# Performance work log

Measured on AMD Instinct MI355X. Metric: run time of the kernel, lower is better.

Reference implementation:

```python
import jax, jax.numpy as jnp
import numpy as np

R = 3           # disp_range = (3, 3)
DU = 2 * R + 1  # 7 displacements per axis, 49 total
PNAMES = ['mn_w1','mn_b1','mn_w2','mn_b2','mn_w3','mn_b3','mn_w4','mn_b4','mn_wd','mn_bd','mn_w5','mn_b5','dap_w','dap_b','me_w1','me_b1','me_w2','me_b2','me_w3','me_b3','gz1_w','gz1_b','gr1_w','gr1_b','gq1_w','gq1_b','gz2_w','gz2_b','gr2_w','gr2_b','gq2_w','gq2_b','fh_w1','fh_b1','fh_w2','fh_b2']


def conv2d(x, w, b, stride=(1, 1), padding=((1, 1), (1, 1))):
    y = jax.lax.conv_general_dilated(x, w, stride, padding, dimension_numbers=('NCHW', 'OIHW', 'NCHW'))
    return y + b[None, :, None, None]


def warp_backwards(f, flow):
    # bilinear backward warp with zero padding; flow[:,0]=u (x offset), flow[:,1]=v (y offset)
    B, C, H, W = f.shape
    gy, gx = jnp.meshgrid(jnp.arange(H, dtype=flow.dtype), jnp.arange(W, dtype=flow.dtype), indexing='ij')
    x = gx[None] + flow[:, 0]
    y = gy[None] + flow[:, 1]
    x0, y0 = jnp.floor(x), jnp.floor(y)
    wx, wy = x - x0, y - y0

    def corner(yy, xx, wgt):
        valid = (yy >= 0) & (yy <= H - 1) & (xx >= 0) & (xx <= W - 1)
        yc = jnp.clip(yy, 0, H - 1).astype(jnp.int32)
        xc = jnp.clip(xx, 0, W - 1).astype(jnp.int32)
        g = jax.vmap(lambda fb, yb, xb: fb[:, yb, xb])(f, yc, xc)  # (B,C,H,W)
        return g * (wgt * valid.astype(f.dtype))[:, None]

    return (corner(y0, x0, (1 - wy) * (1 - wx)) + corner(y0, x0 + 1, (1 - wy) * wx)
            + corner(y0 + 1, x0, wy * (1 - wx)) + corner(y0 + 1, x0 + 1, wy * wx))


def gru_step(h, x, wz, bz, wr, br, wq, bq, pad):
    hx = jnp.concatenate([h, x], axis=1)
    z = jax.nn.sigmoid(conv2d(hx, wz, bz, padding=pad))
    r = jax.nn.sigmoid(conv2d(hx, wr, br, padding=pad))
    q = jnp.tanh(conv2d(jnp.concatenate([r * h, x], axis=1), wq, bq, padding=pad))
    return (1.0 - z) * h + z * q


def _run(fmap1, fmap2, h, flow, P):
    B, C, H, W = fmap1.shape
    lrelu, relu = jax.nn.leaky_relu, jax.nn.relu
    # backward warp of fmap2 by current (detached) flow
    f2w = warp_backwards(fmap2, jax.lax.stop_gradient(flow))
    # --- correlation volume: 49 zero-padded shifts of warped fmap2, paired with fmap1 ---
    pad2 = jnp.pad(f2w, ((0, 0), (0, 0), (R, R), (R, R)))
    # k = i*DU + j  <->  shift (di, dj) = (i-R, j-R); shifted[...,y,x] = f2w[y+dj, x+di]
    shifted = jnp.stack([pad2[:, :, j:j + H, i:i + W] for i in range(DU) for j in range(DU)], axis=1)  # (B,49,C,H,W)
    valid = (jnp.sum(shifted, axis=2, keepdims=True) != 0).astype(fmap1.dtype)
    mvol = jnp.concatenate([jnp.broadcast_to(fmap1[:, None], shifted.shape), shifted], axis=2) * valid  # (B,49,2C,H,W)
    # --- matching net, applied per displacement ---
    x = mvol.reshape(B * DU * DU, 2 * C, H, W)
    x = relu(conv2d(x, P['mn_w1'], P['mn_b1']))
    x = relu(conv2d(x, P['mn_w2'], P['mn_b2'], stride=(2, 2)))
    x = relu(conv2d(x, P['mn_w3'], P['mn_b3']))
    x = relu(conv2d(x, P['mn_w4'], P['mn_b4']))
    # ConvTranspose2d(k=4, s=2, p=1) == lhs-dilated conv with pad 2
    x = jax.lax.conv_general_dilated(x, P['mn_wd'], (1, 1), ((2, 2), (2, 2)), lhs_dilation=(2, 2), dimension_numbers=('NCHW', 'OIHW', 'NCHW')) + P['mn_bd'][None, :, None, None]
    x = relu(x)
    x = conv2d(x, P['mn_w5'], P['mn_b5'])  # (B*49, 1, H, W)
    cvol = x.reshape(B, DU * DU, H, W)
    # --- displacement-aware projection: 1x1 conv across the 49 displacement channels ---
    cvol = jnp.einsum('ok,bkhw->bohw', P['dap_w'], cvol) + P['dap_b'][None, :, None, None]
    # --- motion encoder ---
    m = jnp.concatenate([cvol, fmap1, flow], axis=1)  # (B, 49+C+2, H, W)
    m = lrelu(conv2d(m, P['me_w1'], P['me_b1']))
    m = lrelu(conv2d(m, P['me_w2'], P['me_b2']))
    m = conv2d(m, P['me_w3'], P['me_b3'])             # (B, 94, H, W)
    xg = jnp.concatenate([m, flow], axis=1)           # (B, 96, H, W)
    # --- separable conv GRU: horizontal (1x5) then vertical (5x1) pass ---
    h = gru_step(h, xg, P['gz1_w'], P['gz1_b'], P['gr1_w'], P['gr1_b'], P['gq1_w'], P['gq1_b'], ((0, 0), (2, 2)))
    h = gru_step(h, xg, P['gz2_w'], P['gz2_b'], P['gr2_w'], P['gr2_b'], P['gq2_w'], P['gq2_b'], ((2, 2), (0, 0)))
    # --- flow head: softmax over 49 displacements, expectation of displacement grid ---
    s = lrelu(jnp.einsum('oi,bihw->bohw', P['fh_w1'], h) + P['fh_b1'][None, :, None, None])
    s = lrelu(jnp.einsum('oi,bihw->bohw', P['fh_w2'], s) + P['fh_b2'][None, :, None, None])
    prob = jax.nn.softmax(s, axis=1)  # (B, 49, H, W)
    dr = jnp.arange(-R, R + 1, dtype=fmap1.dtype)
    disp = jnp.stack([jnp.broadcast_to(dr[:, None], (DU, DU)), jnp.broadcast_to(dr[None, :], (DU, DU))], axis=0).reshape(2, DU * DU)
    d = jnp.einsum('bkhw,ck->bchw', prob, disp)
    return h, flow + d


def _params(key):
    shapes = {'mn_w1': (96, 64, 3, 3), 'mn_b1': (96,), 'mn_w2': (128, 96, 3, 3), 'mn_b2': (128,), 'mn_w3': (128, 128, 3, 3), 'mn_b3': (128,), 'mn_w4': (64, 128, 3, 3), 'mn_b4': (64,), 'mn_wd': (32, 64, 4, 4), 'mn_bd': (32,), 'mn_w5': (1, 32, 3, 3), 'mn_b5': (1,), 'dap_w': (49, 49), 'dap_b': (49,), 'me_w1': (128, 83, 3, 3), 'me_b1': (128,), 'me_w2': (128, 128, 3, 3), 'me_b2': (128,), 'me_w3': (94, 128, 3, 3), 'me_b3': (94,), 'gz1_w': (128, 224, 1, 5), 'gz1_b': (128,), 'gr1_w': (128, 224, 1, 5), 'gr1_b': (128,), 'gq1_w': (128, 224, 1, 5), 'gq1_b': (128,), 'gz2_w': (128, 224, 5, 1), 'gz2_b': (128,), 'gr2_w': (128, 224, 5, 1), 'gr2_b': (128,), 'gq2_w': (128, 224, 5, 1), 'gq2_b': (128,), 'fh_w1': (256, 128), 'fh_b1': (256,), 'fh_w2': (49, 256), 'fh_b2': (49,)}
    keys = jax.random.split(key, len(shapes))
    return {n: jax.random.normal(k, s, dtype=jnp.float32) * 0.05 for (n, s), k in zip(shapes.items(), keys)}


def setup_inputs():
    key = jax.random.key(0)
    k1, k2, k3, k4, kp = jax.random.split(key, 5)
    B, C, H, W, HID = 2, 32, 64, 96, 128
    inp = {'fmap1': jax.random.normal(k1, (B, C, H, W), jnp.float32),
           'fmap2': jax.random.normal(k2, (B, C, H, W), jnp.float32),
           'h': jax.random.normal(k3, (B, HID, H, W), jnp.float32),
           'flow': jax.random.normal(k4, (B, 2, H, W), jnp.float32),
           'i': 0}
    inp.update(_params(kp))
    return inp


def reference(fmap1, fmap2, h, flow, mn_w1, mn_b1, mn_w2, mn_b2, mn_w3, mn_b3, mn_w4, mn_b4, mn_wd, mn_bd, mn_w5, mn_b5, dap_w, dap_b, me_w1, me_b1, me_w2, me_b2, me_w3, me_b3, gz1_w, gz1_b, gr1_w, gr1_b, gq1_w, gq1_b, gz2_w, gz2_b, gr2_w, gr2_b, gq2_w, gq2_b, fh_w1, fh_b1, fh_w2, fh_b2, i):
    ps = (mn_w1, mn_b1, mn_w2, mn_b2, mn_w3, mn_b3, mn_w4, mn_b4, mn_wd, mn_bd, mn_w5, mn_b5, dap_w, dap_b, me_w1, me_b1, me_w2, me_b2, me_w3, me_b3, gz1_w, gz1_b, gr1_w, gr1_b, gq1_w, gq1_b, gz2_w, gz2_b, gr2_w, gr2_b, gq2_w, gq2_b, fh_w1, fh_b1, fh_w2, fh_b2)
    return _run(fmap1, fmap2, h, flow, dict(zip(PNAMES, ps)))
```

## Files before the change

### kernel.cpp

```cpp
#include <hip/hip_runtime.h>
#include <math.h>

typedef unsigned short u16;
typedef unsigned int u32;
typedef __attribute__((ext_vector_type(8))) short bf16x8;
typedef __attribute__((ext_vector_type(4))) float f32x4;

#define HWW 6144

__device__ __forceinline__ float sigmoidf_(float x) { return 1.f / (1.f + expf(-x)); }
__device__ __forceinline__ float lrelu_(float x) { return x >= 0.f ? x : 0.01f * x; }
__device__ __forceinline__ u16 f2bf(float f) {
    u32 u = __float_as_uint(f);
    u += 0x7fffu + ((u >> 16) & 1u);
    return (u16)(u >> 16);
}
__device__ __forceinline__ float bf2f(u16 h) { return __uint_as_float(((u32)h) << 16); }
__device__ __forceinline__ u32 pk2(float a, float b) { return (u32)f2bf(a) | ((u32)f2bf(b) << 16); }

struct WJob { const float* src; unsigned long dstOff; int OC, rowOff, IC, ICP, NT; unsigned long cum; };
struct WJobs { WJob j[16]; long total; };

__global__ __launch_bounds__(256) void k_wt_all(WJobs J, u16* __restrict__ base)
{
    long i = (long)blockIdx.x * 256 + threadIdx.x;
    if (i >= J.total) return;
    int jb = 0;
    #pragma unroll
    for (int k = 1; k < 16; ++k) if (i >= (long)J.j[k].cum) jb = k;
    WJob w = J.j[jb];
    long local = i - (long)w.cum;
    int c = (int)(local % w.ICP);
    int t = (int)((local / w.ICP) % w.NT);
    int o = (int)(local / ((long)w.ICP * w.NT));
    float val = (c < w.IC) ? w.src[((long)o * w.IC + c) * w.NT + t] : 0.f;
    base[w.dstOff + ((long)(w.rowOff + o) * w.NT + t) * w.ICP + c] = f2bf(val);
}

__global__ __launch_bounds__(256) void k_wt_dq(const float* __restrict__ w, u16* __restrict__ dst)
{
    int i = blockIdx.x * 256 + threadIdx.x;
    if (i >= 32768) return;
    int c = i & 63; int t = (i >> 6) & 3; int o = (i >> 8) & 31; int q = i >> 13;
    int ry = q >> 1, rx = q & 1, ta = t >> 1, tb = t & 1;
    int ky = ry + 2 * ta, kx = rx + 2 * tb;
    float val = w[(((long)o * 64 + c) * 4 + ky) * 4 + kx];
    dst[(long)q * 8192 + o * 256 + t * 64 + c] = f2bf(val);
}

__global__ __launch_bounds__(256) void k_wt5(const float* __restrict__ w, float* __restrict__ wt)
{
    int i = blockIdx.x * 256 + threadIdx.x;
    if (i >= 288) return;
    int t = i % 9, c = i / 9;
    wt[t * 32 + c] = w[c * 9 + t];
}

__global__ void k_catb(const float* __restrict__ a, const float* __restrict__ b, float* __restrict__ d)
{
    int i = threadIdx.x;
    if (i < 128) d[i] = a[i];
    else if (i < 256) d[i] = b[i - 128];
}

__global__ __launch_bounds__(256) void k_prep_f1(const float* __restrict__ fmap1, u16* __restrict__ f1bf)
{
    int gid = blockIdx.x * 256 + threadIdx.x;
    if (gid >= 24576) return;
    int idx = gid >> 1, half = gid & 1;
    int b = idx / HWW, p = idx % HWW;
    const float* fb = fmap1 + (long)b * 32 * HWW + p + (long)(half * 16) * HWW;
    u32 pk[8];
    #pragma unroll
    for (int c2 = 0; c2 < 8; ++c2)
        pk[c2] = pk2(fb[(long)(2 * c2) * HWW], fb[(long)(2 * c2 + 1) * HWW]);
    u16* op = f1bf + ((long)idx << 5) + half * 16;
    ((uint4*)op)[0] = make_uint4(pk[0], pk[1], pk[2], pk[3]);
    ((uint4*)op)[1] = make_uint4(pk[4], pk[5], pk[6], pk[7]);
}

__global__ __launch_bounds__(256) void k_warp(const float* __restrict__ fmap2, const float* __restrict__ flow,
                                              u16* __restrict__ f2wbf, float* __restrict__ cs)
{
    int gid = blockIdx.x * 256 + threadIdx.x;
    if (gid >= 24576) return;
    int idx = gid >> 1, half = gid & 1;
    int b = idx / HWW, p = idx % HWW, y = p / 96, x = p % 96;
    float u = flow[(b * 2 + 0) * HWW + p], v = flow[(b * 2 + 1) * HWW + p];
    float fx = (float)x + u, fy = (float)y + v;
    float fx0 = floorf(fx), fy0 = floorf(fy);
    float wx = fx - fx0, wy = fy - fy0;
    int x0 = (int)fx0, y0i = (int)fy0, x1 = x0 + 1, y1 = y0i + 1;
    bool vx0 = x0 >= 0 && x0 < 96, vx1 = x1 >= 0 && x1 < 96;
    bool vy0 = y0i >= 0 && y0i < 64, vy1 = y1 >= 0 && y1 < 64;
    float m00 = (vy0 && vx0) ? (1.f - wy) * (1.f - wx) : 0.f;
    float m01 = (vy0 && vx1) ? (1.f - wy) * wx : 0.f;
    float m10 = (vy1 && vx0) ? wy * (1.f - wx) : 0.f;
    float m11 = (vy1 && vx1) ? wy * wx : 0.f;
    int cx0 = min(max(x0, 0), 95), cx1 = min(max(x1, 0), 95);
    int cy0 = min(max(y0i, 0), 63), cy1 = min(max(y1, 0), 63);
    int i00 = cy0 * 96 + cx0, i01 = cy0 * 96 + cx1, i10 = cy1 * 96 + cx0, i11 = cy1 * 96 + cx1;
    const float* fb = fmap2 + (long)b * 32 * HWW + (long)(half * 16) * HWW;
    float s = 0.f; u32 pk[8];
    #pragma unroll
    for (int c2 = 0; c2 < 8; ++c2) {
        const float* fa = fb + (long)(2 * c2) * HWW;
        const float* fc = fb + (long)(2 * c2 + 1) * HWW;
        float g0 = m00 * fa[i00] + m01 * fa[i01] + m10 * fa[i10] + m11 * fa[i11];
        float g1 = m00 * fc[i00] + m01 * fc[i01] + m10 * fc[i10] + m11 * fc[i11];
        s += g0 + g1;
        pk[c2] = pk2(g0, g1);
    }
    u16* op = f2wbf + ((long)idx << 5) + half * 16;
    ((uint4*)op)[0] = make_uint4(pk[0], pk[1], pk[2], pk[3]);
    ((uint4*)op)[1] = make_uint4(pk[4], pk[5], pk[6], pk[7]);
    float stot = s + __shfl_xor(s, 1);
    if (half == 0) cs[idx] = stot;
}

template<int BM, int BN, int MODE, int KH, int KW, int PH, int PW, int STRIDE, int ACT, int OUTF32,
         int IH, int IW, int OH, int OW, int ICP, int NKT>
__global__ __launch_bounds__(256) void k_gemm(
    const u16* __restrict__ A0, const u16* __restrict__ A1,
    const float* __restrict__ csm, const u16* __restrict__ Wb,
    const float* __restrict__ bias,
    u16* __restrict__ outb, u16* __restrict__ outb2, float* __restrict__ outf,
    int OC, int ldc, int coff, int nOff)
{
    constexpr int WAVES_M = (BM == 64) ? 2 : ((BN == 128) ? 2 : 4);
    constexpr int WAVES_N = 4 / WAVES_M;
    constexpr int WTM = BM / WAVES_M;
    constexpr int WTN = BN / WAVES_N;
    constexpr int MF = WTM / 16;
    constexpr int NF = WTN / 16;
    constexpr int LDR = 40;
    __shared__ u16 As[2][BM * LDR];
    __shared__ u16 Bs[2][BN * LDR];
    int tid = threadIdx.x;
    constexpr int ATHR = 256 / BM;
    int mrow = tid / ATHR;
    int khOff = (tid % ATHR) * (32 / ATHR);
    int gmS = blockIdx.x * BM + mrow;

    constexpr int OHW = (MODE == 1) ? 6144 : ((MODE == 2) ? 1536 : OH * OW);
    constexpr int OWW = (MODE == 1) ? 96 : ((MODE == 2) ? 48 : OW);
    int nImg = gmS / OHW;
    int rem = gmS - nImg * OHW;
    int y0 = rem / OWW, x0 = rem - y0 * OWW;

    int ryz = 0, rxz = 0, diS = 0, djS = 0, bImgHWW = 0;
    u32 vmask = 0;
    const u16* Arow = A0;
    if (MODE == 0) {
        Arow = A0 + ((long)nImg * IH * IW + (long)y0 * STRIDE * IW + (long)x0 * STRIDE) * ICP + khOff;
    } else if (MODE == 1) {
        int n = nOff + nImg;
        int bImg = n / 49; int kd = n - bImg * 49;
        diS = kd / 7 - 3; djS = kd % 7 - 3;
        bImgHWW = bImg * HWW;
        #pragma unroll
        for (int t = 0; t < 9; ++t) {
            int dy = t / 3 - 1, dx = t % 3 - 1;
            int yy = y0 + dy, xx = x0 + dx, ys = yy + djS, xs = xx + diS;
            bool v = yy >= 0 && yy < 64 && xx >= 0 && xx < 96 && ys >= 0 && ys < 64 && xs >= 0 && xs < 96;
            if (v) v = (csm[bImgHWW + ys * 96 + xs] != 0.f);
            vmask |= (v ? 1u : 0u) << t;
        }
    } else {
        ryz = blockIdx.z >> 1; rxz = blockIdx.z & 1;
    }
    const u16* WbZ = Wb + (MODE == 2 ? (long)blockIdx.z * 32 * 256 : 0);
    int n0 = blockIdx.y * BN;

    auto loadTile = [&](int kt, uint4& va0, uint4& va1) {
        va0 = make_uint4(0u, 0u, 0u, 0u); va1 = make_uint4(0u, 0u, 0u, 0u);
        if (MODE == 0) {
            constexpr int KTC = ICP / 32;
            int t = kt / KTC;
            int c0 = (kt - t * KTC) << 5;
            int dy = t / KW - PH, dx = t - (t / KW) * KW - PW;
            int iy = y0 * STRIDE + dy, ix = x0 * STRIDE + dx;
            if (iy >= 0 && iy < IH && ix >= 0 && ix < IW) {
                const u16* sp = Arow + (long)(dy * IW + dx) * ICP + c0;
                va0 = *(const uint4*)sp;
                if (BM == 128) va1 = *(const uint4*)(sp + 8);
            }
        } else if (MODE == 1) {
            int t = kt >> 1, half = kt & 1;
            if ((vmask >> t) & 1u) {
                int dy = t / 3 - 1, dx = t % 3 - 1;
                int yy = y0 + dy, xx = x0 + dx;
                const u16* sp = half ? (A1 + (((long)bImgHWW + (yy + djS) * 96 + (xx + diS)) << 5) + khOff)
                                     : (A0 + (((long)bImgHWW + yy * 96 + xx) << 5) + khOff);
                va0 = *(const uint4*)sp;
                if (BM == 128) va1 = *(const uint4*)(sp + 8);
            }
        } else {
            int t = kt >> 1, c0 = (kt & 1) << 5;
            int ta = t >> 1, tb = t & 1;
            int iy = y0 + ryz + ta - 1, ix = x0 + rxz + tb - 1;
            if (iy >= 0 && iy < 32 && ix >= 0 && ix < 48) {
                const u16* sp = A0 + (((long)(nImg * 32 + iy) * 48 + ix) << 6) + c0 + khOff;
                va0 = *(const uint4*)sp;
                if (BM == 128) va1 = *(const uint4*)(sp + 8);
            }
        }
    };
    auto writeA = [&](int bufn, const uint4& va0, const uint4& va1) {
        *(uint4*)&As[bufn][mrow * LDR + khOff] = va0;
        if (BM == 128) *(uint4*)&As[bufn][mrow * LDR + khOff + 8] = va1;
    };

    bool bldr = (tid < 2 * BN);
    int brow = tid >> 1, ko = (tid & 1) << 4;
    const u16* Bp = WbZ + (long)(n0 + brow) * (NKT * 32) + ko;
    auto loadB = [&](int kt, uint4& vb0, uint4& vb1) {
        const u16* wp = Bp + (long)kt * 32;
        vb0 = *(const uint4*)wp; vb1 = *(const uint4*)(wp + 8);
    };
    auto writeB = [&](int bufn, const uint4& vb0, const uint4& vb1) {
        *(uint4*)&Bs[bufn][brow * LDR + ko] = vb0;
        *(uint4*)&Bs[bufn][brow * LDR + ko + 8] = vb1;
    };

    int lane = tid & 63, wid = tid >> 6;
    int wm = (WAVES_N == 2) ? (wid >> 1) : wid;
    int wn = (WAVES_N == 2) ? (wid & 1) : 0;
    int fr = lane & 15, fg = lane >> 4;
    f32x4 acc[MF][NF];
    #pragma unroll
    for (int i = 0; i < MF; ++i)
        #pragma unroll
        for (int j = 0; j < NF; ++j)
            acc[i][j] = (f32x4){0.f, 0.f, 0.f, 0.f};

    uint4 pa0, pa1, pb0, pb1;
    {
        uint4 t0, t1;
        loadTile(0, t0, t1);
        writeA(0, t0, t1);
        if (bldr) { uint4 u0, u1; loadB(0, u0, u1); writeB(0, u0, u1); }
    }
    if (NKT > 1) {
        loadTile(1, pa0, pa1);
        if (bldr) loadB(1, pb0, pb1);
    }
    __syncthreads();

    #pragma unroll
    for (int kt = 0; kt < NKT; ++kt) {
        int cur = kt & 1;
        uint4 qa0, qa1, qb0, qb1;
        if (kt + 2 < NKT) {
            loadTile(kt + 2, qa0, qa1);
            if (bldr) loadB(kt + 2, qb0, qb1);
        }
        bf16x8 af[MF], bfv[NF];
        #pragma unroll
        for (int i = 0; i < MF; ++i)
            af[i] = *(const bf16x8*)&As[cur][(wm * WTM + i * 16 + fr) * LDR + fg * 8];
        #pragma unroll
        for (int j = 0; j < NF; ++j)
            bfv[j] = *(const bf16x8*)&Bs[cur][(wn * WTN + j * 16 + fr) * LDR + fg * 8];
        #pragma unroll
        for (int i = 0; i < MF; ++i)
            #pragma unroll
            for (int j = 0; j < NF; ++j)
                acc[i][j] = __builtin_amdgcn_mfma_f32_16x16x32_bf16(af[i], bfv[j], acc[i][j], 0, 0, 0);
        if (kt + 1 < NKT) {
            int bufn = cur ^ 1;
            writeA(bufn, pa0, pa1);
            if (bldr) writeB(bufn, pb0, pb1);
            __syncthreads();
            pa0 = qa0; pa1 = qa1; pb0 = qb0; pb1 = qb1;
        }
    }

    #pragma unroll
    for (int i = 0; i < MF; ++i) {
        #pragma unroll
        for (int j = 0; j < NF; ++j) {
            int nn = n0 + wn * WTN + j * 16 + fr;
            if (nn >= OC) continue;
            #pragma unroll
            for (int rr = 0; rr < 4; ++rr) {
                int mloc = wm * WTM + i * 16 + fg * 4 + rr;
                long gm = (long)blockIdx.x * BM + mloc;
                float v = acc[i][j][rr] + bias[nn];
                if (ACT == 1) v = fmaxf(v, 0.f);
                else if (ACT == 2) v = lrelu_(v);
                if (OUTF32) {
                    outf[gm * ldc + coff + nn] = v;
                } else if (MODE == 2) {
                    int nI = (int)(gm / 1536); int rq = (int)(gm - (long)nI * 1536);
                    int Y = rq / 48, X = rq - (rq / 48) * 48;
                    long di = (((long)nI * 64 + 2 * Y + ryz) * 96 + (2 * X + rxz)) * 32 + nn;
                    outb[di] = f2bf(v);
                } else {
                    long di = gm * ldc + coff + nn;
                    u16 hv = f2bf(v);
                    outb[di] = hv;
                    if (outb2) outb2[di] = hv;
                }
            }
        }
    }
}

__global__ __launch_bounds__(256) void k_conv5n(const u16* __restrict__ x5, const float* __restrict__ w5t,
                                                const float* __restrict__ b5, u16* __restrict__ cvolT,
                                                int N, int n0)
{
    int idx = blockIdx.x * 256 + threadIdx.x;
    if (idx >= N * HWW) return;
    int nl = idx / HWW, p = idx % HWW, y = p / 96, x = p % 96;
    float acc = b5[0];
    #pragma unroll
    for (int t = 0; t < 9; ++t) {
        int iy = y + t / 3 - 1, ix = x + t % 3 - 1;
        if (iy < 0 || iy >= 64 || ix < 0 || ix >= 96) continue;
        const u16* sp = x5 + (((long)nl * HWW + iy * 96 + ix) << 5);
        const float* wt_ = w5t + t * 32;
        #pragma unroll
        for (int c8 = 0; c8 < 4; ++c8) {
            uint4 v = *(const uint4*)(sp + c8 * 8);
            acc = fmaf(bf2f((u16)(v.x & 0xffffu)), wt_[c8 * 8 + 0], acc);
            acc = fmaf(bf2f((u16)(v.x >> 16)),     wt_[c8 * 8 + 1], acc);
            acc = fmaf(bf2f((u16)(v.y & 0xffffu)), wt_[c8 * 8 + 2], acc);
            acc = fmaf(bf2f((u16)(v.y >> 16)),     wt_[c8 * 8 + 3], acc);
            acc = fmaf(bf2f((u16)(v.z & 0xffffu)), wt_[c8 * 8 + 4], acc);
            acc = fmaf(bf2f((u16)(v.z >> 16)),     wt_[c8 * 8 + 5], acc);
            acc = fmaf(bf2f((u16)(v.w & 0xffffu)), wt_[c8 * 8 + 6], acc);
            acc = fmaf(bf2f((u16)(v.w >> 16)),     wt_[c8 * 8 + 7], acc);
        }
    }
    int n = n0 + nl;
    int b = n / 49, k = n - b * 49;
    cvolT[((long)b * HWW + p) * 64 + k] = f2bf(acc);
}

__global__ __launch_bounds__(256) void k_me_tail(const float* __restrict__ fmap1, const float* __restrict__ flow,
                                                 u16* __restrict__ mein)
{
    int gid = blockIdx.x * 256 + threadIdx.x;
    if (gid >= 73728) return;
    int j = gid / 12288, idx = gid - j * 12288;
    int b = idx / HWW, p = idx % HWW;
    int c0 = 49 + j * 8;
    u16* mp = mein + (long)idx * 96;
    #pragma unroll
    for (int q = 0; q < 8; ++q) {
        int c = c0 + q;
        if (c >= 96) break;
        float v;
        if (c < 81) v = fmap1[((long)(b * 32 + (c - 49))) * HWW + p];
        else if (c == 81) v = flow[(b * 2 + 0) * HWW + p];
        else if (c == 82) v = flow[(b * 2 + 1) * HWW + p];
        else v = 0.f;
        mp[c] = f2bf(v);
    }
}

__global__ __launch_bounds__(256) void k_set_head(const float* __restrict__ h, const float* __restrict__ flow,
                                                  float* __restrict__ hst, u16* __restrict__ hx,
                                                  u16* __restrict__ hx2)
{
    int gid = blockIdx.x * 256 + threadIdx.x;
    if (gid >= 49152) return;
    int cq = gid / 12288, idx = gid - cq * 12288;
    int b = idx / HWW, p = idx % HWW;
    int c0 = cq * 32;
    const float* hp = h + (long)b * 128 * HWW + p;
    float* hs = hst + (long)idx * 128;
    u16* hxp = hx + (long)idx * 224;
    #pragma unroll
    for (int c = c0; c < c0 + 32; c += 8) {
        float v[8];
        #pragma unroll
        for (int q = 0; q < 8; ++q) v[q] = hp[(long)(c + q) * HWW];
        *(float4*)&hs[c] = make_float4(v[0], v[1], v[2], v[3]);
        *(float4*)&hs[c + 4] = make_float4(v[4], v[5], v[6], v[7]);
        uint4 pk = make_uint4(pk2(v[0], v[1]), pk2(v[2], v[3]), pk2(v[4], v[5]), pk2(v[6], v[7]));
        *(uint4*)&hxp[c] = pk;
    }
    if (cq == 0) {
        u16 uu = f2bf(flow[(b * 2 + 0) * HWW + p]);
        u16 vv = f2bf(flow[(b * 2 + 1) * HWW + p]);
        long o = (long)idx * 224;
        hx[o + 222] = uu; hx[o + 223] = vv;
        hx2[o + 222] = uu; hx2[o + 223] = vv;
    }
}

__global__ __launch_bounds__(256) void k_post_zr(const float* __restrict__ azr, const float* __restrict__ hst,
                                                 float* __restrict__ z, u16* __restrict__ hx2)
{
    int gid = blockIdx.x * 256 + threadIdx.x;
    if (gid >= 49152) return;
    int cq = gid / 12288, idx = gid - cq * 12288;
    int c0 = cq * 32;
    const float* ap = azr + (long)idx * 256;
    const float* hs = hst + (long)idx * 128;
    float* zp = z + (long)idx * 128;
    u16* xp = hx2 + (long)idx * 224;
    #pragma unroll
    for (int c = c0; c < c0 + 32; c += 8) {
        float4 a0 = *(const float4*)&ap[c], a1 = *(const float4*)&ap[c + 4];
        float4 r0 = *(const float4*)&ap[128 + c], r1 = *(const float4*)&ap[128 + c + 4];
        float4 h0 = *(const float4*)&hs[c], h1v = *(const float4*)&hs[c + 4];
        float z0 = sigmoidf_(a0.x), z1 = sigmoidf_(a0.y), z2 = sigmoidf_(a0.z), z3 = sigmoidf_(a0.w);
        float z4 = sigmoidf_(a1.x), z5 = sigmoidf_(a1.y), z6 = sigmoidf_(a1.z), z7 = sigmoidf_(a1.w);
        *(float4*)&zp[c] = make_float4(z0, z1, z2, z3);
        *(float4*)&zp[c + 4] = make_float4(z4, z5, z6, z7);
        float rh0 = sigmoidf_(r0.x) * h0.x, rh1 = sigmoidf_(r0.y) * h0.y;
        float rh2 = sigmoidf_(r0.z) * h0.z, rh3 = sigmoidf_(r0.w) * h0.w;
        float rh4 = sigmoidf_(r1.x) * h1v.x, rh5 = sigmoidf_(r1.y) * h1v.y;
        float rh6 = sigmoidf_(r1.z) * h1v.z, rh7 = sigmoidf_(r1.w) * h1v.w;
        uint4 pk = make_uint4(pk2(rh0, rh1), pk2(rh2, rh3), pk2(rh4, rh5), pk2(rh6, rh7));
        *(uint4*)&xp[c] = pk;
    }
}

template<int FIN>
__global__ __launch_bounds__(256) void k_post_q(const float* __restrict__ aq, const float* __restrict__ z,
                                                const float* __restrict__ hst, float* __restrict__ h1f,
                                                u16* __restrict__ hxdst, float* __restrict__ outH)
{
    int gid = blockIdx.x * 256 + threadIdx.x;
    if (gid >= 49152) return;
    int cq = gid / 12288, idx = gid - cq * 12288;
    int b = idx / HWW, p = idx % HWW;
    int c0 = cq * 32;
    const float* ap = aq + (long)idx * 128;
    const float* zp = z + (long)idx * 128;
    const float* hs = hst + (long)idx * 128;
    #pragma unroll
    for (int c = c0; c < c0 + 32; c += 8) {
        float hn[8];
        #pragma unroll
        for (int q = 0; q < 8; ++q) {
            float qq = tanhf(ap[c + q]);
            float zv = zp[c + q];
            hn[q] = (1.f - zv) * hs[c + q] + zv * qq;
        }
        uint4 pk = make_uint4(pk2(hn[0], hn[1]), pk2(hn[2], hn[3]), pk2(hn[4], hn[5]), pk2(hn[6], hn[7]));
        if (FIN == 0) {
            *(float4*)&h1f[(long)idx * 128 + c] = make_float4(hn[0], hn[1], hn[2], hn[3]);
            *(float4*)&h1f[(long)idx * 128 + c + 4] = make_float4(hn[4], hn[5], hn[6], hn[7]);
            *(uint4*)&hxdst[(long)idx * 224 + c] = pk;
        } else {
            #pragma unroll
            for (int q = 0; q < 8; ++q)
                outH[((long)(b * 128 + c + q)) * HWW + p] = hn[q];
            *(uint4*)&hxdst[(long)idx * 128 + c] = pk;
        }
    }
}

__global__ __launch_bounds__(256) void k_soft(const float* __restrict__ s2, const float* __restrict__ flow,
                                              float* __restrict__ outFlow)
{
    int idx = blockIdx.x * 256 + threadIdx.x;
    if (idx >= 12288) return;
    int b = idx / HWW, p = idx % HWW;
    const float* sp = s2 + (long)idx * 64;
    float lg[49];
    #pragma unroll
    for (int k = 0; k < 48; k += 4) {
        float4 v = *(const float4*)&sp[k];
        lg[k] = v.x; lg[k + 1] = v.y; lg[k + 2] = v.z; lg[k + 3] = v.w;
    }
    lg[48] = sp[48];
    float m = -1e30f;
    #pragma unroll
    for (int k = 0; k < 49; ++k) m = fmaxf(m, lg[k]);
    float s = 0.f, a0 = 0.f, a1 = 0.f;
    #pragma unroll
    for (int k = 0; k < 49; ++k) {
        float e = expf(lg[k] - m);
        s += e;
        a0 += e * (float)(k / 7 - 3);
        a1 += e * (float)(k % 7 - 3);
    }
    float inv = 1.f / s;
    outFlow[(long)(b * 2 + 0) * HWW + p] = flow[(long)(b * 2 + 0) * HWW + p] + a0 * inv;
    outFlow[(long)(b * 2 + 1) * HWW + p] = flow[(long)(b * 2 + 1) * HWW + p] + a1 * inv;
}

extern "C" void kernel_launch(void* const* d_in, const int* in_sizes, int n_in,
                              void* d_out, int out_size, void* d_ws, size_t ws_size,
                              hipStream_t stream)
{
    const float* fmap1 = (const float*)d_in[0];
    const float* fmap2 = (const float*)d_in[1];
    const float* h     = (const float*)d_in[2];
    const float* flow  = (const float*)d_in[3];
    int pb = (in_sizes[4] == 1) ? 5 : 4;
    const float* mn_w1 = (const float*)d_in[pb + 0];
    const float* mn_b1 = (const float*)d_in[pb + 1];
    const float* mn_w2 = (const float*)d_in[pb + 2];
    const float* mn_b2 = (const float*)d_in[pb + 3];
    const float* mn_w3 = (const float*)d_in[pb + 4];
    const float* mn_b3 = (const float*)d_in[pb + 5];
    const float* mn_w4 = (const float*)d_in[pb + 6];
    const float* mn_b4 = (const float*)d_in[pb + 7];
    const float* mn_wd = (const float*)d_in[pb + 8];
    const float* mn_bd = (const float*)d_in[pb + 9];
    const float* mn_w5 = (const float*)d_in[pb + 10];
    const float* mn_b5 = (const float*)d_in[pb + 11];
    const float* dap_w = (const float*)d_in[pb + 12];
    const float* dap_b = (const float*)d_in[pb + 13];
    const float* me_w1 = (const float*)d_in[pb + 14];
    const float* me_b1 = (const float*)d_in[pb + 15];
    const float* me_w2 = (const float*)d_in[pb + 16];
    const float* me_b2 = (const float*)d_in[pb + 17];
    const float* me_w3 = (const float*)d_in[pb + 18];
    const float* me_b3 = (const float*)d_in[pb + 19];
    const float* gz1_w = (const float*)d_in[pb + 20];
    const float* gz1_b = (const float*)d_in[pb + 21];
    const float* gr1_w = (const float*)d_in[pb + 22];
    const float* gr1_b = (const float*)d_in[pb + 23];
    const float* gq1_w = (const float*)d_in[pb + 24];
    const float* gq1_b = (const float*)d_in[pb + 25];
    const float* gz2_w = (const float*)d_in[pb + 26];
    const float* gz2_b = (const float*)d_in[pb + 27];
    const float* gr2_w = (const float*)d_in[pb + 28];
    const float* gr2_b = (const float*)d_in[pb + 29];
    const float* gq2_w = (const float*)d_in[pb + 30];
    const float* gq2_b = (const float*)d_in[pb + 31];
    const float* fh_w1 = (const float*)d_in[pb + 32];
    const float* fh_b1 = (const float*)d_in[pb + 33];
    const float* fh_w2 = (const float*)d_in[pb + 34];
    const float* fh_b2 = (const float*)d_in[pb + 35];

    char* wsB = (char*)d_ws;
    size_t off = 0;
    auto alc = [&](size_t bytes) { size_t o = off; off = (off + bytes + 255) & ~(size_t)255; return o; };

    size_t o_wc1  = alc(128 * 576 * 2);
    size_t o_wc2  = alc(128 * 864 * 2);
    size_t o_wc3  = alc((size_t)128 * 1152 * 2);
    size_t o_wc4  = alc((size_t)64 * 1152 * 2);
    size_t o_wdq  = alc(32768 * 2);
    size_t o_wme1 = alc(128 * 864 * 2);
    size_t o_wme2 = alc((size_t)128 * 1152 * 2);
    size_t o_wme3 = alc((size_t)128 * 1152 * 2);
    size_t o_wzr1 = alc((size_t)256 * 1120 * 2);
    size_t o_wq1  = alc((size_t)128 * 1120 * 2);
    size_t o_wzr2 = alc((size_t)256 * 1120 * 2);
    size_t o_wq2  = alc((size_t)128 * 1120 * 2);
    size_t o_wfh1 = alc(256 * 128 * 2);
    size_t o_wfh2 = alc(64 * 256 * 2);
    size_t o_wdapb= alc(64 * 64 * 2);
    size_t o_w5t  = alc(288 * 4);
    size_t o_bzr1 = alc(256 * 4);
    size_t o_bzr2 = alc(256 * 4);
    size_t wArenaBytes = off;

    size_t o_f1bf = alc((size_t)12288 * 32 * 2);
    size_t o_f2wb = alc((size_t)12288 * 32 * 2);
    size_t o_cs   = alc(12288 * 4);
    size_t o_cvolT= alc((size_t)12288 * 64 * 2);

    const int CH = 49;
    size_t sharedBase = off;
    size_t offA = sharedBase;
    auto alcA = [&](size_t bytes) { size_t o = offA; offA = (offA + bytes + 255) & ~(size_t)255; return o; };
    size_t o_x1 = alcA((size_t)CH * 6144 * 96 * 2);
    size_t o_x2 = alcA((size_t)98 * 1536 * 128 * 2);
    size_t o_x3 = alcA((size_t)98 * 1536 * 128 * 2);
    size_t o_x4 = alcA((size_t)98 * 1536 * 64 * 2);
    size_t o_x5 = alcA((size_t)98 * 6144 * 32 * 2);
    size_t offB2 = sharedBase;
    auto alcB = [&](size_t bytes) { size_t o = offB2; offB2 = (offB2 + bytes + 255) & ~(size_t)255; return o; };
    size_t o_mein = alcB((size_t)12288 * 96 * 2);
    size_t o_m1   = alcB((size_t)12288 * 128 * 2);
    size_t o_m2   = alcB((size_t)12288 * 128 * 2);
    size_t o_hx   = alcB((size_t)12288 * 224 * 2);
    size_t o_hx2  = alcB((size_t)12288 * 224 * 2);
    size_t o_h2bf = alcB((size_t)12288 * 128 * 2);
    size_t o_s1b  = alcB((size_t)12288 * 256 * 2);
    size_t o_hst  = alcB((size_t)12288 * 128 * 4);
    size_t o_h1f  = alcB((size_t)12288 * 128 * 4);
    size_t o_zf   = alcB((size_t)12288 * 128 * 4);
    size_t o_azr  = alcB((size_t)12288 * 256 * 4);
    size_t o_aqf  = alcB((size_t)12288 * 128 * 4);
    size_t o_s2   = alcB((size_t)12288 * 64 * 4);

    u16* wbase = (u16*)wsB;
    u16* wdq  = (u16*)(wsB + o_wdq);
    float* w5t = (float*)(wsB + o_w5t);
    float* bzr1 = (float*)(wsB + o_bzr1);
    float* bzr2 = (float*)(wsB + o_bzr2);
    u16* wc1  = (u16*)(wsB + o_wc1);   u16* wc2  = (u16*)(wsB + o_wc2);
    u16* wc3  = (u16*)(wsB + o_wc3);   u16* wc4  = (u16*)(wsB + o_wc4);
    u16* wme1 = (u16*)(wsB + o_wme1);  u16* wme2 = (u16*)(wsB + o_wme2);
    u16* wme3 = (u16*)(wsB + o_wme3);
    u16* wzr1 = (u16*)(wsB + o_wzr1);  u16* wq1  = (u16*)(wsB + o_wq1);
    u16* wzr2 = (u16*)(wsB + o_wzr2);  u16* wq2  = (u16*)(wsB + o_wq2);
    u16* wfh1 = (u16*)(wsB + o_wfh1);  u16* wfh2 = (u16*)(wsB + o_wfh2);
    u16* wdapb= (u16*)(wsB + o_wdapb);

    u16* f1bf = (u16*)(wsB + o_f1bf);  u16* f2wb = (u16*)(wsB + o_f2wb);
    float* cs = (float*)(wsB + o_cs);
    u16* cvolT = (u16*)(wsB + o_cvolT);
    u16* x1 = (u16*)(wsB + o_x1); u16* x2 = (u16*)(wsB + o_x2); u16* x3 = (u16*)(wsB + o_x3);
    u16* x4 = (u16*)(wsB + o_x4); u16* x5 = (u16*)(wsB + o_x5);
    u16* mein = (u16*)(wsB + o_mein);
    u16* m1 = (u16*)(wsB + o_m1); u16* m2 = (u16*)(wsB + o_m2);
    u16* hx = (u16*)(wsB + o_hx); u16* hx2 = (u16*)(wsB + o_hx2);
    u16* h2bf = (u16*)(wsB + o_h2bf);  u16* s1b = (u16*)(wsB + o_s1b);
    float* hst = (float*)(wsB + o_hst); float* h1f = (float*)(wsB + o_h1f);
    float* zf = (float*)(wsB + o_zf); float* azr = (float*)(wsB + o_azr);
    float* aqf = (float*)(wsB + o_aqf); float* s2 = (float*)(wsB + o_s2);

    float* outH = (float*)d_out;
    float* outFlow = outH + (long)2 * 128 * HWW;

    auto nb = [](long total, int bs) { return (unsigned)((total + bs - 1) / bs); };

    hipMemsetAsync(wsB, 0, wArenaBytes, stream);
    hipMemsetAsync(wsB + o_cvolT, 0, (size_t)12288 * 64 * 2, stream);

    WJobs J;
    {
        auto mk = [](const float* src, size_t dstOffBytes, int OC, int rowOff, int IC, int ICP, int NT) {
            WJob w; w.src = src; w.dstOff = dstOffBytes / 2; w.OC = OC; w.rowOff = rowOff;
            w.IC = IC; w.ICP = ICP; w.NT = NT; w.cum = 0; return w;
        };
        J.j[0]  = mk(mn_w1, o_wc1, 96, 0, 64, 64, 9);
        J.j[1]  = mk(mn_w2, o_wc2, 128, 0, 96, 96, 9);
        J.j[2]  = mk(mn_w3, o_wc3, 128, 0, 128, 128, 9);
        J.j[3]  = mk(mn_w4, o_wc4, 64, 0, 128, 128, 9);
        J.j[4]  = mk(me_w1, o_wme1, 128, 0, 83, 96, 9);
        J.j[5]  = mk(me_w2, o_wme2, 128, 0, 128, 128, 9);
        J.j[6]  = mk(me_w3, o_wme3, 94, 0, 128, 128, 9);
        J.j[7]  = mk(gz1_w, o_wzr1, 128, 0, 224, 224, 5);
        J.j[8]  = mk(gr1_w, o_wzr1, 128, 128, 224, 224, 5);
        J.j[9]  = mk(gq1_w, o_wq1, 128, 0, 224, 224, 5);
        J.j[10] = mk(gz2_w, o_wzr2, 128, 0, 224, 224, 5);
        J.j[11] = mk(gr2_w, o_wzr2, 128, 128, 224, 224, 5);
        J.j[12] = mk(gq2_w, o_wq2, 128, 0, 224, 224, 5);
        J.j[13] = mk(fh_w1, o_wfh1, 256, 0, 128, 128, 1);
        J.j[14] = mk(fh_w2, o_wfh2, 49, 0, 256, 256, 1);
        J.j[15] = mk(dap_w, o_wdapb, 49, 0, 49, 64, 1);
        long cum = 0;
        for (int k = 0; k < 16; ++k) {
            J.j[k].cum = cum;
            cum += (long)J.j[k].OC * J.j[k].NT * J.j[k].ICP;
        }
        J.total = cum;
    }
    k_wt_all<<<nb(J.total, 256), 256, 0, stream>>>(J, wbase);
    k_wt_dq<<<nb(32768, 256), 256, 0, stream>>>(mn_wd, wdq);
    k_wt5<<<2, 256, 0, stream>>>(mn_w5, w5t);
    k_catb<<<1, 256, 0, stream>>>(gz1_b, gr1_b, bzr1);
    k_catb<<<1, 256, 0, stream>>>(gz2_b, gr2_b, bzr2);

    k_prep_f1<<<nb(24576, 256), 256, 0, stream>>>(fmap1, f1bf);
    k_warp<<<nb(24576, 256), 256, 0, stream>>>(fmap2, flow, f2wb, cs);

    for (int n0 = 0; n0 < 98; n0 += CH) {
        k_gemm<128,128,1,3,3,1,1,1,1,0,64,96,64,96,32,18><<<dim3(2352, 1), 256, 0, stream>>>(
            f1bf, f2wb, cs, wc1, mn_b1, x1, nullptr, nullptr, 96, 96, 0, n0);
        k_gemm<128,128,0,3,3,1,1,2,1,0,64,96,32,48,96,27><<<dim3(588, 1), 256, 0, stream>>>(
            x1, nullptr, nullptr, wc2, mn_b2, x2 + (long)n0 * 196608, nullptr, nullptr, 128, 128, 0, 0);
    }
    k_gemm<128,128,0,3,3,1,1,1,1,0,32,48,32,48,128,36><<<dim3(1176, 1), 256, 0, stream>>>(
        x2, nullptr, nullptr, wc3, mn_b3, x3, nullptr, nullptr, 128, 128, 0, 0);
    k_gemm<128,64,0,3,3,1,1,1,1,0,32,48,32,48,128,36><<<dim3(1176, 1), 256, 0, stream>>>(
        x3, nullptr, nullptr, wc4, mn_b4, x4, nullptr, nullptr, 64, 64, 0, 0);
    k_gemm<128,32,2,4,4,2,2,1,1,0,32,48,32,48,64,8><<<dim3(1176, 1, 4), 256, 0, stream>>>(
        x4, nullptr, nullptr, wdq, mn_bd, x5, nullptr, nullptr, 32, 32, 0, 0);
    k_conv5n<<<nb(98L * HWW, 256), 256, 0, stream>>>(x5, w5t, mn_b5, cvolT, 98, 0);

    k_gemm<64,64,0,1,1,0,0,1,0,0,64,96,64,96,64,2><<<dim3(192, 1), 256, 0, stream>>>(
        cvolT, nullptr, nullptr, wdapb, dap_b, mein, nullptr, nullptr, 49, 96, 0, 0);
    k_me_tail<<<nb(73728, 256), 256, 0, stream>>>(fmap1, flow, mein);

    k_gemm<64,128,0,3,3,1,1,1,2,0,64,96,64,96,96,27><<<dim3(192, 1), 256, 0, stream>>>(
        mein, nullptr, nullptr, wme1, me_b1, m1, nullptr, nullptr, 128, 128, 0, 0);
    k_gemm<64,128,0,3,3,1,1,1,2,0,64,96,64,96,128,36><<<dim3(192, 1), 256, 0, stream>>>(
        m1, nullptr, nullptr, wme2, me_b2, m2, nullptr, nullptr, 128, 128, 0, 0);
    k_gemm<64,128,0,3,3,1,1,1,0,0,64,96,64,96,128,36><<<dim3(192, 1), 256, 0, stream>>>(
        m2, nullptr, nullptr, wme3, me_b3, hx, hx2, nullptr, 94, 224, 128, 0);

    k_set_head<<<nb(49152, 256), 256, 0, stream>>>(h, flow, hst, hx, hx2);
    k_gemm<64,128,0,1,5,0,2,1,0,1,64,96,64,96,224,35><<<dim3(192, 2), 256, 0, stream>>>(
        hx, nullptr, nullptr, wzr1, bzr1, nullptr, nullptr, azr, 256, 256, 0, 0);
    k_post_zr<<<nb(49152, 256), 256, 0, stream>>>(azr, hst, zf, hx2);
    k_gemm<64,128,0,1,5,0,2,1,0,1,64,96,64,96,224,35><<<dim3(192, 1), 256, 0, stream>>>(
        hx2, nullptr, nullptr, wq1, gq1_b, nullptr, nullptr, aqf, 128, 128, 0, 0);
    k_post_q<0><<<nb(49152, 256), 256, 0, stream>>>(aqf, zf, hst, h1f, hx, nullptr);

    k_gemm<64,128,0,5,1,2,0,1,0,1,64,96,64,96,224,35><<<dim3(192, 2), 256, 0, stream>>>(
        hx, nullptr, nullptr, wzr2, bzr2, nullptr, nullptr, azr, 256, 256, 0, 0);
    k_post_zr<<<nb(49152, 256), 256, 0, stream>>>(azr, h1f, zf, hx2);
    k_gemm<64,128,0,5,1,2,0,1,0,1,64,96,64,96,224,35><<<dim3(192, 1), 256, 0, stream>>>(
        hx2, nullptr, nullptr, wq2, gq2_b, nullptr, nullptr, aqf, 128, 128, 0, 0);
    k_post_q<1><<<nb(49152, 256), 256, 0, stream>>>(aqf, zf, h1f, nullptr, h2bf, outH);

    k_gemm<64,128,0,1,1,0,0,1,2,0,64,96,64,96,128,4><<<dim3(192, 2), 256, 0, stream>>>(
        h2bf, nullptr, nullptr, wfh1, fh_b1, s1b, nullptr, nullptr, 256, 256, 0, 0);
    k_gemm<64,64,0,1,1,0,0,1,2,1,64,96,64,96,256,8><<<dim3(192, 1), 256, 0, stream>>>(
        s1b, nullptr, nullptr, wfh2, fh_b2, nullptr, nullptr, s2, 49, 64, 0, 0);
    k_soft<<<nb(12288, 256), 256, 0, stream>>>(s2, flow, outFlow);
}
```

Baseline: 761.0 us.

## Load GEMM weight fragments straight to registers; run full correlation batch in one launch

The B (weight) operand in the MFMA GEMM is no longer staged through shared memory. Each wave now reads its bf16x8 fragments directly from global memory into registers, prefetched one k-step ahead. The A-tile prefetch distance drops from two steps to one, which reduces register pressure but hides less load latency. Separately, the two-chunk loop over the 98 correlation channels is replaced by single full-size launches of the first two motion-net convolutions, enlarging the x1 scratch buffer. The goal is to cut LDS traffic, free shared memory for occupancy, and reduce launch count, at the cost of more scattered global weight loads per wave.

```diff
diff --git a/kernel.cpp b/kernel.cpp
--- a/kernel.cpp
+++ b/kernel.cpp
@@ -135,7 +135,6 @@
     constexpr int NF = WTN / 16;
     constexpr int LDR = 40;
     __shared__ u16 As[2][BM * LDR];
-    __shared__ u16 Bs[2][BN * LDR];
     int tid = threadIdx.x;
     constexpr int ATHR = 256 / BM;
     int mrow = tid / ATHR;
@@ -211,22 +210,18 @@
         if (BM == 128) *(uint4*)&As[bufn][mrow * LDR + khOff + 8] = va1;
     };
 
-    bool bldr = (tid < 2 * BN);
-    int brow = tid >> 1, ko = (tid & 1) << 4;
-    const u16* Bp = WbZ + (long)(n0 + brow) * (NKT * 32) + ko;
-    auto loadB = [&](int kt, uint4& vb0, uint4& vb1) {
-        const u16* wp = Bp + (long)kt * 32;
-        vb0 = *(const uint4*)wp; vb1 = *(const uint4*)(wp + 8);
-    };
-    auto writeB = [&](int bufn, const uint4& vb0, const uint4& vb1) {
-        *(uint4*)&Bs[bufn][brow * LDR + ko] = vb0;
-        *(uint4*)&Bs[bufn][brow * LDR + ko + 8] = vb1;
-    };
-
     int lane = tid & 63, wid = tid >> 6;
     int wm = (WAVES_N == 2) ? (wid >> 1) : wid;
     int wn = (WAVES_N == 2) ? (wid & 1) : 0;
     int fr = lane & 15, fg = lane >> 4;
+
+    const u16* BpL[NF];
+    #pragma unroll
+    for (int j = 0; j < NF; ++j) {
+        int rowB = n0 + wn * WTN + j * 16 + fr;
+        BpL[j] = WbZ + (long)rowB * (NKT * 32) + fg * 8;
+    }
+
     f32x4 acc[MF][NF];
     #pragma unroll
     for (int i = 0; i < MF; ++i)
@@ -234,45 +229,40 @@
         for (int j = 0; j < NF; ++j)
             acc[i][j] = (f32x4){0.f, 0.f, 0.f, 0.f};
 
-    uint4 pa0, pa1, pb0, pb1;
+    bf16x8 bcur[NF], bnxt[NF];
     {
         uint4 t0, t1;
         loadTile(0, t0, t1);
         writeA(0, t0, t1);
-        if (bldr) { uint4 u0, u1; loadB(0, u0, u1); writeB(0, u0, u1); }
-    }
-    if (NKT > 1) {
-        loadTile(1, pa0, pa1);
-        if (bldr) loadB(1, pb0, pb1);
+        #pragma unroll
+        for (int j = 0; j < NF; ++j) bcur[j] = *(const bf16x8*)(BpL[j]);
     }
     __syncthreads();
 
     #pragma unroll
     for (int kt = 0; kt < NKT; ++kt) {
         int cur = kt & 1;
-        uint4 qa0, qa1, qb0, qb1;
-        if (kt + 2 < NKT) {
-            loadTile(kt + 2, qa0, qa1);
-            if (bldr) loadB(kt + 2, qb0, qb1);
-        }
-        bf16x8 af[MF], bfv[NF];
+        uint4 na0, na1;
+        if (kt + 1 < NKT) {
+            loadTile(kt + 1, na0, na1);
+            #pragma unroll
+            for (int j = 0; j < NF; ++j) bnxt[j] = *(const bf16x8*)(BpL[j] + (kt + 1) * 32);
+        }
+        bf16x8 af[MF];
         #pragma unroll
         for (int i = 0; i < MF; ++i)
             af[i] = *(const bf16x8*)&As[cur][(wm * WTM + i * 16 + fr) * LDR + fg * 8];
-        #pragma unroll
-        for (int j = 0; j < NF; ++j)
-            bfv[j] = *(const bf16x8*)&Bs[cur][(wn * WTN + j * 16 + fr) * LDR + fg * 8];
         #pragma unroll
         for (int i = 0; i < MF; ++i)
             #pragma unroll
             for (int j = 0; j < NF; ++j)
-                acc[i][j] = __builtin_amdgcn_mfma_f32_16x16x32_bf16(af[i], bfv[j], acc[i][j], 0, 0, 0);
+                acc[i][j] = __builtin_amdgcn_mfma_f32_16x16x32_bf16(af[i], bcur[j], acc[i][j], 0, 0, 0);
         if (kt + 1 < NKT) {
             int bufn = cur ^ 1;
-            writeA(bufn, pa0, pa1);
-            if (bldr) writeB(bufn, pb0, pb1);
+            writeA(bufn, na0, na1);
+            #pragma unroll
+            for (int j = 0; j < NF; ++j) bcur[j] = bnxt[j];
             __syncthreads();
-            pa0 = qa0; pa1 = qa1; pb0 = qb0; pb1 = qb1;
         }
     }
 
@@ -562,11 +552,10 @@
     size_t o_cs   = alc(12288 * 4);
     size_t o_cvolT= alc((size_t)12288 * 64 * 2);
 
-    const int CH = 49;
     size_t sharedBase = off;
     size_t offA = sharedBase;
     auto alcA = [&](size_t bytes) { size_t o = offA; offA = (offA + bytes + 255) & ~(size_t)255; return o; };
-    size_t o_x1 = alcA((size_t)CH * 6144 * 96 * 2);
+    size_t o_x1 = alcA((size_t)98 * 6144 * 96 * 2);
     size_t o_x2 = alcA((size_t)98 * 1536 * 128 * 2);
     size_t o_x3 = alcA((size_t)98 * 1536 * 128 * 2);
     size_t o_x4 = alcA((size_t)98 * 1536 * 64 * 2);
@@ -660,12 +649,10 @@
     k_prep_f1<<<nb(24576, 256), 256, 0, stream>>>(fmap1, f1bf);
     k_warp<<<nb(24576, 256), 256, 0, stream>>>(fmap2, flow, f2wb, cs);
 
-    for (int n0 = 0; n0 < 98; n0 += CH) {
-        k_gemm<128,128,1,3,3,1,1,1,1,0,64,96,64,96,32,18><<<dim3(2352, 1), 256, 0, stream>>>(
-            f1bf, f2wb, cs, wc1, mn_b1, x1, nullptr, nullptr, 96, 96, 0, n0);
-        k_gemm<128,128,0,3,3,1,1,2,1,0,64,96,32,48,96,27><<<dim3(588, 1), 256, 0, stream>>>(
-            x1, nullptr, nullptr, wc2, mn_b2, x2 + (long)n0 * 196608, nullptr, nullptr, 128, 128, 0, 0);
-    }
+    k_gemm<128,128,1,3,3,1,1,1,1,0,64,96,64,96,32,18><<<dim3(4704, 1), 256, 0, stream>>>(
+        f1bf, f2wb, cs, wc1, mn_b1, x1, nullptr, nullptr, 96, 96, 0, 0);
+    k_gemm<128,128,0,3,3,1,1,2,1,0,64,96,32,48,96,27><<<dim3(1176, 1), 256, 0, stream>>>(
+        x1, nullptr, nullptr, wc2, mn_b2, x2, nullptr, nullptr, 128, 128, 0, 0);
     k_gemm<128,128,0,3,3,1,1,1,1,0,32,48,32,48,128,36><<<dim3(1176, 1), 256, 0, stream>>>(
         x2, nullptr, nullptr, wc3, mn_b3, x3, nullptr, nullptr, 128, 128, 0, 0);
     k_gemm<128,64,0,3,3,1,1,1,1,0,32,48,32,48,128,36><<<dim3(1176, 1), 256, 0, stream>>>(
```

Measured after the change: 886.1 us. 16.4% more time.
